# Kernel optimization log

Hardware: AMD Instinct MI355X
Metric: run time of the kernel (lower is better)

Reference implementation:

```python
import jax, jax.numpy as jnp
import numpy as np
import math

D = 256        # input_size == d_k == d_v (per the module: d_k = input_size)
H = 4          # n_heads
MAX_LEN = 800  # PositionalEncoding max_len
NEG = float(-(2**32) + 1)
LN_EPS = 1e-5


def _make_pe():
    pe = np.zeros((MAX_LEN, D), dtype=np.float32)
    pos = np.arange(MAX_LEN, dtype=np.float32)[:, None]
    div = np.exp(np.arange(0, D, 2, dtype=np.float32) * -(math.log(10000.0) / D))
    pe[:, 0::2] = np.sin(pos * div)
    pe[:, 1::2] = np.cos(pos * div)
    return jnp.asarray(pe)


def setup_inputs() -> dict:
    key = jax.random.key(0)
    ks = jax.random.split(key, 12)
    B, L = 32, 512

    def xavier(k, shape):
        fan_in, fan_out = shape[0], shape[1]
        std = math.sqrt(2.0 / (fan_in + fan_out))
        return jax.random.normal(k, shape, dtype=jnp.float32) * std

    return {
        "Q": jax.random.normal(ks[0], (B, L, D), dtype=jnp.float32),
        "K": jax.random.normal(ks[1], (B, L, D), dtype=jnp.float32),
        "V": jax.random.normal(ks[2], (B, L, D), dtype=jnp.float32),
        "mask": jax.random.randint(ks[3], (B, L), 0, 2).astype(jnp.bool_),
        "pe": _make_pe(),
        "W_q": xavier(ks[4], (D, H * D)),
        "W_k": xavier(ks[5], (D, H * D)),
        "W_v": xavier(ks[6], (D, H * D)),
        "W_o": xavier(ks[7], (H * D, D)),
        "w1": xavier(ks[8], (D, D)),
        "b1": jnp.zeros((D,), dtype=jnp.float32),
        "w2": xavier(ks[9], (D, D)),
        "b2": jnp.zeros((D,), dtype=jnp.float32),
        "gamma": jnp.ones((D,), dtype=jnp.float32),
        "beta": jnp.zeros((D,), dtype=jnp.float32),
    }


def _layer_norm(x, gamma, beta):
    mu = jnp.mean(x, axis=-1, keepdims=True)
    var = jnp.mean(jnp.square(x - mu), axis=-1, keepdims=True)
    return (x - mu) * jax.lax.rsqrt(var + LN_EPS) * gamma + beta


def _mha(Q, K, V, mask, W_q, W_k, W_v, W_o):
    B, Lq, _ = Q.shape
    Lk = K.shape[1]

    def split_heads(X, W, L):
        # (B, L, D) @ (D, H*D) -> (B*H, L, D)
        return (X @ W).reshape(B, L, H, D).transpose(0, 2, 1, 3).reshape(B * H, L, D)

    Qh = split_heads(Q, W_q, Lq)
    Kh = split_heads(K, W_k, Lk)
    Vh = split_heads(V, W_v, Lk)

    scale = D ** 0.5 + 1e-6
    scores = jnp.einsum('bqd,bkd->bqk', Qh, Kh) / scale  # (B*H, Lq, Lk)

    pad = jnp.broadcast_to(mask[:, None, :], (B, H, Lq)).reshape(B * H, Lq)
    pad_mask = jnp.broadcast_to(pad[:, :, None], (B * H, Lq, Lk))
    causal = jnp.triu(jnp.ones((Lq, Lk), dtype=jnp.bool_), k=1)
    full_mask = causal[None] | pad_mask
    scores = jnp.where(full_mask, NEG, scores)

    att = jax.nn.softmax(scores, axis=-1)
    Vatt = jnp.einsum('bqk,bkd->bqd', att, Vh)  # (B*H, Lq, D)
    Vatt = Vatt.reshape(B, H, Lq, D).transpose(0, 2, 1, 3).reshape(B, Lq, H * D)
    return Vatt @ W_o


def reference(Q, K, V, mask, pe, W_q, W_k, W_v, W_o, w1, b1, w2, b2, gamma, beta):
    Lq, Lk, Lv = Q.shape[1], K.shape[1], V.shape[1]
    Qp = Q + pe[None, :Lq]
    Kp = K + pe[None, :Lk]
    Vp = V + pe[None, :Lv]

    Vatt = _mha(Qp, Kp, Vp, mask, W_q, W_k, W_v, W_o)
    X = _layer_norm(Qp + Vatt, gamma, beta)
    ffn = jax.nn.relu(X @ w1.T + b1) @ w2.T + b2
    return _layer_norm(ffn + X, gamma, beta)
```

## Files before the change

kernel.cpp:

```cpp
#include <hip/hip_runtime.h>
#include <stdint.h>

#define SEQ   512
#define DM    256
#define NB    32
#define NH    4
#define HD    (NH * DM)
#define PE_MASK (SEQ * DM - 1)
#define NEGV  (-4294967295.0f)

typedef __attribute__((ext_vector_type(8))) short short8;
typedef __attribute__((ext_vector_type(4))) float f32x4;

#if defined(__has_builtin)
#if __has_builtin(__builtin_amdgcn_global_load_lds)
#define HAS_ASYNC 1
#endif
#endif
#ifndef HAS_ASYNC
#define HAS_ASYNC 0
#endif

__device__ __forceinline__ float b2f(unsigned short u) {
    return __uint_as_float(((uint32_t)u) << 16);
}
__device__ __forceinline__ unsigned short f2b(float f) {
    uint32_t u = __float_as_uint(f);
    u += 0x7fffu + ((u >> 16) & 1u);
    return (unsigned short)(u >> 16);
}

__global__ __launch_bounds__(256) void mask_canon(
    const unsigned char* __restrict__ raw, int* __restrict__ canon)
{
    __shared__ int enc_byte, enc_odd;
    int tid = threadIdx.x;
    if (tid == 0) { enc_byte = 0; enc_odd = 0; }
    __syncthreads();
    if (tid < 255 && raw[tid * 4 + 1]) atomicOr(&enc_byte, 1);
    if (tid < 128 && ((const int*)raw)[tid * 2 + 1]) atomicOr(&enc_odd, 1);
    __syncthreads();
    int i = blockIdx.x * 256 + tid;
    int v;
    if (enc_byte)      v = (raw[i] != 0);
    else if (enc_odd)  v = (((const int*)raw)[i] != 0);
    else               v = ((((const int*)raw)[i * 2] | ((const int*)raw)[i * 2 + 1]) != 0);
    canon[i] = v;
}

__global__ __launch_bounds__(256) void addpe3(
    const float* __restrict__ Q, const float* __restrict__ K,
    const float* __restrict__ V, const float* __restrict__ pe,
    unsigned short* __restrict__ Qp, unsigned short* __restrict__ Kp,
    unsigned short* __restrict__ Vp)
{
    int blk = blockIdx.x;
    int seg = blk >> 12;
    const float* X = (seg == 0) ? Q : (seg == 1) ? K : V;
    unsigned short* O = (seg == 0) ? Qp : (seg == 1) ? Kp : Vp;
    long i = (long)((blk & 4095) * 256 + threadIdx.x) * 4;
    float4 x = *reinterpret_cast<const float4*>(X + i);
    float4 p = *reinterpret_cast<const float4*>(pe + (i & PE_MASK));
    ushort4 o;
    o.x = f2b(x.x + p.x); o.y = f2b(x.y + p.y);
    o.z = f2b(x.z + p.z); o.w = f2b(x.w + p.w);
    *reinterpret_cast<ushort4*>(O + i) = o;
}

__global__ __launch_bounds__(256) void conv2(
    const float* __restrict__ w1, const float* __restrict__ w2,
    unsigned short* __restrict__ o1, unsigned short* __restrict__ o2)
{
    int blk = blockIdx.x;
    const float* in = (blk < 64) ? w1 : w2;
    unsigned short* out = (blk < 64) ? o1 : o2;
    long i = (long)((blk & 63) * 256 + threadIdx.x) * 4;
    float4 x = *reinterpret_cast<const float4*>(in + i);
    ushort4 o;
    o.x = f2b(x.x); o.y = f2b(x.y); o.z = f2b(x.z); o.w = f2b(x.w);
    *reinterpret_cast<ushort4*>(out + i) = o;
}

__global__ __launch_bounds__(256) void transpose_f2b3(
    const float* __restrict__ in0, const float* __restrict__ in1,
    const float* __restrict__ in2, unsigned short* __restrict__ out,
    int ldin, int ldout, long outStride)
{
    int z = blockIdx.z;
    const float* in = (z == 0) ? in0 : (z == 1) ? in1 : in2;
    unsigned short* op = out + z * outStride;
    __shared__ unsigned short tile[32][33];
    int r0 = blockIdx.y * 32, c0 = blockIdx.x * 32;
    int i = threadIdx.x >> 3;
    int j = (threadIdx.x & 7) * 4;
    float4 v = *reinterpret_cast<const float4*>(in + (long)(r0 + i) * ldin + c0 + j);
    tile[i][j + 0] = f2b(v.x); tile[i][j + 1] = f2b(v.y);
    tile[i][j + 2] = f2b(v.z); tile[i][j + 3] = f2b(v.w);
    __syncthreads();
    ushort4 w;
    w.x = tile[j + 0][i]; w.y = tile[j + 1][i]; w.z = tile[j + 2][i]; w.w = tile[j + 3][i];
    *reinterpret_cast<ushort4*>(op + (long)(c0 + i) * ldout + r0 + j) = w;
}

__global__ __launch_bounds__(256) void transpose_f2b(
    const float* __restrict__ in, unsigned short* __restrict__ out,
    int ldin, int ldout)
{
    __shared__ unsigned short tile[32][33];
    int r0 = blockIdx.y * 32, c0 = blockIdx.x * 32;
    int i = threadIdx.x >> 3;
    int j = (threadIdx.x & 7) * 4;
    float4 v = *reinterpret_cast<const float4*>(in + (long)(r0 + i) * ldin + c0 + j);
    tile[i][j + 0] = f2b(v.x); tile[i][j + 1] = f2b(v.y);
    tile[i][j + 2] = f2b(v.z); tile[i][j + 3] = f2b(v.w);
    __syncthreads();
    ushort4 w;
    w.x = tile[j + 0][i]; w.y = tile[j + 1][i]; w.z = tile[j + 2][i]; w.w = tile[j + 3][i];
    *reinterpret_cast<ushort4*>(out + (long)(c0 + i) * ldout + r0 + j) = w;
}

__global__ __launch_bounds__(256) void transpose_bf16(
    const unsigned short* __restrict__ in, unsigned short* __restrict__ out,
    int ldin, int ldout, long sInB, long sInH, long sOutB, long sOutH, int Hdiv)
{
    int z = blockIdx.z; int b = z / Hdiv; int h = z % Hdiv;
    const unsigned short* ip = in + b * sInB + h * sInH;
    unsigned short* op = out + b * sOutB + h * sOutH;
    __shared__ unsigned short tile[32][33];
    int r0 = blockIdx.y * 32, c0 = blockIdx.x * 32;
    int i = threadIdx.x >> 3;
    int j = (threadIdx.x & 7) * 4;
    ushort4 v = *reinterpret_cast<const ushort4*>(ip + (long)(r0 + i) * ldin + c0 + j);
    tile[i][j + 0] = v.x; tile[i][j + 1] = v.y; tile[i][j + 2] = v.z; tile[i][j + 3] = v.w;
    __syncthreads();
    ushort4 w;
    w.x = tile[j + 0][i]; w.y = tile[j + 1][i]; w.z = tile[j + 2][i]; w.w = tile[j + 3][i];
    *reinterpret_cast<ushort4*>(op + (long)(c0 + i) * ldout + r0 + j) = w;
}

template<bool BIAS, bool RELU, bool OUTBF16>
__global__ __launch_bounds__(256) void gemm_bt(
    const unsigned short* __restrict__ A, int lda,
    const unsigned short* __restrict__ B, int ldb,
    void* __restrict__ Cv, int ldc,
    const float* __restrict__ bias, float scale, int K, int Hdiv,
    long sAb, long sAh, long sAz,
    long sBb, long sBh, long sBz,
    long sCb, long sCh, long sCz)
{
    const int m0 = blockIdx.y * 128;
    const int n0 = blockIdx.x * 128;
    int z  = blockIdx.z;
    int bb = z / Hdiv, hh = z % Hdiv;
    const unsigned short* Ab = A + bb * sAb + hh * sAh + (long)z * sAz;
    const unsigned short* Bb = B + bb * sBb + hh * sBh + (long)z * sBz;
    long coff = bb * sCb + hh * sCh + (long)z * sCz;

    __shared__ unsigned short As[128 * 32];
    __shared__ unsigned short Bs[128 * 32];

    const int tid  = threadIdx.x;
    const int lane = tid & 63;
    const int wave = tid >> 6;
    const int wm   = (wave >> 1) * 64;
    const int wn   = (wave & 1) * 64;
    const int lm   = lane & 15;
    const int kq   = (lane >> 4) * 8;

    f32x4 acc[4][4] = {};

    for (int k0 = 0; k0 < K; k0 += 32) {
#pragma unroll
        for (int it = 0; it < 2; ++it) {
            int id = tid + it * 256;
            int r  = id >> 2;
            int c8 = (id & 3) * 8;
            const unsigned short* gA = Ab + (long)(m0 + r) * lda + k0 + c8;
            const unsigned short* gB = Bb + (long)(n0 + r) * ldb + k0 + c8;
#if HAS_ASYNC
            unsigned short* lA = &As[(size_t)(it * 256 + wave * 64) * 8];
            unsigned short* lB = &Bs[(size_t)(it * 256 + wave * 64) * 8];
            __builtin_amdgcn_global_load_lds(
                (const __attribute__((address_space(1))) void*)gA,
                (__attribute__((address_space(3))) void*)lA, 16, 0, 0);
            __builtin_amdgcn_global_load_lds(
                (const __attribute__((address_space(1))) void*)gB,
                (__attribute__((address_space(3))) void*)lB, 16, 0, 0);
#else
            *reinterpret_cast<uint4*>(&As[(size_t)id * 8]) =
                *reinterpret_cast<const uint4*>(gA);
            *reinterpret_cast<uint4*>(&Bs[(size_t)id * 8]) =
                *reinterpret_cast<const uint4*>(gB);
#endif
        }
        __syncthreads();

        short8 af[4], bfr[4];
#pragma unroll
        for (int i = 0; i < 4; ++i)
            af[i] = *reinterpret_cast<const short8*>(&As[(wm + i * 16 + lm) * 32 + kq]);
#pragma unroll
        for (int j = 0; j < 4; ++j)
            bfr[j] = *reinterpret_cast<const short8*>(&Bs[(wn + j * 16 + lm) * 32 + kq]);
#pragma unroll
        for (int i = 0; i < 4; ++i)
#pragma unroll
            for (int j = 0; j < 4; ++j)
                acc[i][j] = __builtin_amdgcn_mfma_f32_16x16x32_bf16(af[i], bfr[j], acc[i][j], 0, 0, 0);
        __syncthreads();
    }

#pragma unroll
    for (int j = 0; j < 4; ++j) {
        int col  = n0 + wn + j * 16 + lm;
        float bv = 0.f;
        if (BIAS) bv = bias[col];
#pragma unroll
        for (int i = 0; i < 4; ++i) {
#pragma unroll
            for (int r = 0; r < 4; ++r) {
                int row = m0 + wm + i * 16 + (lane >> 4) * 4 + r;
                float v = acc[i][j][r] * scale + bv;
                if (RELU) v = fmaxf(v, 0.f);
                long idx = coff + (long)row * ldc + col;
                if (OUTBF16) reinterpret_cast<unsigned short*>(Cv)[idx] = f2b(v);
                else         reinterpret_cast<float*>(Cv)[idx] = v;
            }
        }
    }
}

__global__ __launch_bounds__(256, 3) void flash_attn(
    const unsigned short* __restrict__ Qh,
    const unsigned short* __restrict__ Kh,
    const unsigned short* __restrict__ VhT,
    unsigned short* __restrict__ Vatt,
    const int* __restrict__ maskc, int bh0, float scale, int nbh)
{
    const int tid  = threadIdx.x;
    const int lane = tid & 63;
    const int wave = tid >> 6;
    const int lm   = lane & 15;
    const int qg   = lane >> 4;
    const int kq   = qg * 8;

    const int L = blockIdx.x;
    int z, qt;
    if ((nbh & 7) == 0) {
        int x = L & 7, m = L >> 3;
        qt = m & 7;
        z  = x + 8 * (m >> 3);
    } else {
        z = L % nbh; qt = L / nbh;
    }
    const int b_l = z >> 2, h = z & 3;
    const int m0  = qt * 64;
    const int wq0 = m0 + wave * 16;
    const long qkbase = (long)b_l * SEQ * HD + (long)h * DM;
    const unsigned short* Aq = Qh + qkbase;
    const unsigned short* Ak = Kh + qkbase;
    const unsigned short* Av = VhT + (long)b_l * SEQ * HD + (long)h * SEQ * DM;
    unsigned short* Ov = Vatt + qkbase;
    const int bglob = (bh0 + z) >> 2;

    __shared__ unsigned short Ks[SEQ * 32];
    __shared__ __align__(16) unsigned short Pw[4][16][40];

    f32x4 S[32] = {};
    const int NT = (m0 >> 4) + wave + 1;

    for (int kc = 0; kc < 8; ++kc) {
        for (int it = 0; it <= qt; ++it) {
            int id = tid + it * 256;
            const unsigned short* g = Ak + (long)(id >> 2) * HD + kc * 32 + (id & 3) * 8;
#if HAS_ASYNC
            unsigned short* l = &Ks[(size_t)(it * 256 + wave * 64) * 8];
            __builtin_amdgcn_global_load_lds(
                (const __attribute__((address_space(1))) void*)g,
                (__attribute__((address_space(3))) void*)l, 16, 0, 0);
#else
            *reinterpret_cast<uint4*>(&Ks[(size_t)id * 8]) =
                *reinterpret_cast<const uint4*>(g);
#endif
        }
        short8 qf = *reinterpret_cast<const short8*>(
            Aq + (long)(wq0 + lm) * HD + kc * 32 + kq);
        __syncthreads();
#pragma unroll
        for (int nt = 0; nt < 32; ++nt) {
            if (nt < NT) {
                short8 bf = *reinterpret_cast<const short8*>(&Ks[(nt * 16 + lm) * 32 + kq]);
                S[nt] = __builtin_amdgcn_mfma_f32_16x16x32_bf16(qf, bf, S[nt], 0, 0, 0);
            }
        }
        __syncthreads();
    }

    unsigned short* Vb0 = Ks;
    unsigned short* Vb1 = Ks + 8192;
#pragma unroll
    for (int it = 0; it < 4; ++it) {
        int id = tid + it * 256;
        const unsigned short* g = Av + (long)(id >> 2) * SEQ + (id & 3) * 8;
#if HAS_ASYNC
        unsigned short* l = &Vb0[(size_t)(it * 256 + wave * 64) * 8];
        __builtin_amdgcn_global_load_lds(
            (const __attribute__((address_space(1))) void*)g,
            (__attribute__((address_space(3))) void*)l, 16, 0, 0);
#else
        *reinterpret_cast<uint4*>(&Vb0[(size_t)id * 8]) =
            *reinterpret_cast<const uint4*>(g);
#endif
    }

    int   qrow[4];
    bool  rowm[4];
    float mx[4], sm[4];
#pragma unroll
    for (int r = 0; r < 4; ++r) {
        int q = wq0 + qg * 4 + r;
        qrow[r] = q;
        rowm[r] = maskc[bglob * SEQ + q] != 0;
        mx[r] = -3.4e38f;
    }
#pragma unroll
    for (int nt = 0; nt < 32; ++nt) {
        int k = nt * 16 + lm;
#pragma unroll
        for (int r = 0; r < 4; ++r) {
            float v = S[nt][r] * scale;
            if (k > qrow[r] || rowm[r]) v = NEGV;
            S[nt][r] = v;
            mx[r] = fmaxf(mx[r], v);
        }
    }
#pragma unroll
    for (int r = 0; r < 4; ++r) {
#pragma unroll
        for (int off = 8; off >= 1; off >>= 1)
            mx[r] = fmaxf(mx[r], __shfl_xor(mx[r], off));
        sm[r] = 0.f;
    }
    uint32_t pk[32][2];
#pragma unroll
    for (int nt = 0; nt < 32; ++nt) {
        float e0 = __expf(S[nt][0] - mx[0]);
        float e1 = __expf(S[nt][1] - mx[1]);
        float e2 = __expf(S[nt][2] - mx[2]);
        float e3 = __expf(S[nt][3] - mx[3]);
        sm[0] += e0; sm[1] += e1; sm[2] += e2; sm[3] += e3;
        pk[nt][0] = (uint32_t)f2b(e0) | ((uint32_t)f2b(e1) << 16);
        pk[nt][1] = (uint32_t)f2b(e2) | ((uint32_t)f2b(e3) << 16);
    }
#pragma unroll
    for (int r = 0; r < 4; ++r) {
#pragma unroll
        for (int off = 8; off >= 1; off >>= 1)
            sm[r] += __shfl_xor(sm[r], off);
        sm[r] = 1.0f / sm[r];
    }

    f32x4 O[16] = {};
#pragma unroll
    for (int kc2 = 0; kc2 < 16; ++kc2) {
        unsigned short* Vcur = (kc2 & 1) ? Vb1 : Vb0;
        __syncthreads();
        if (kc2 < 15) {
            unsigned short* Vnext = (kc2 & 1) ? Vb0 : Vb1;
#pragma unroll
            for (int it = 0; it < 4; ++it) {
                int id = tid + it * 256;
                const unsigned short* g =
                    Av + (long)(id >> 2) * SEQ + (kc2 + 1) * 32 + (id & 3) * 8;
#if HAS_ASYNC
                unsigned short* l = &Vnext[(size_t)(it * 256 + wave * 64) * 8];
                __builtin_amdgcn_global_load_lds(
                    (const __attribute__((address_space(1))) void*)g,
                    (__attribute__((address_space(3))) void*)l, 16, 0, 0);
#else
                *reinterpret_cast<uint4*>(&Vnext[(size_t)id * 8]) =
                    *reinterpret_cast<const uint4*>(g);
#endif
            }
        }
#pragma unroll
        for (int t = 0; t < 2; ++t) {
            int nt = kc2 * 2 + t;
#pragma unroll
            for (int r = 0; r < 4; ++r)
                Pw[wave][qg * 4 + r][t * 16 + lm] =
                    (unsigned short)(pk[nt][r >> 1] >> ((r & 1) * 16));
        }
        short8 pf = *reinterpret_cast<const short8*>(&Pw[wave][lm][kq]);
#pragma unroll
        for (int nt2 = 0; nt2 < 16; ++nt2) {
            short8 vf = *reinterpret_cast<const short8*>(&Vcur[(nt2 * 16 + lm) * 32 + kq]);
            O[nt2] = __builtin_amdgcn_mfma_f32_16x16x32_bf16(pf, vf, O[nt2], 0, 0, 0);
        }
    }

#pragma unroll
    for (int nt2 = 0; nt2 < 16; ++nt2) {
#pragma unroll
        for (int r = 0; r < 4; ++r) {
            int l = wq0 + qg * 4 + r;
            Ov[(long)l * HD + nt2 * 16 + lm] = f2b(O[nt2][r] * sm[r]);
        }
    }
}

__global__ __launch_bounds__(256) void ln1_kernel(
    const unsigned short* __restrict__ AttO, const float* __restrict__ Q,
    const float* __restrict__ pe,
    const float* __restrict__ gamma, const float* __restrict__ beta,
    float* __restrict__ outf, unsigned short* __restrict__ outb)
{
    int row  = blockIdx.x * 4 + (threadIdx.x >> 6);
    int lane = threadIdx.x & 63;
    long base = (long)row * DM + lane * 4;
    ushort4 a = *reinterpret_cast<const ushort4*>(AttO + base);
    float4 qv = *reinterpret_cast<const float4*>(Q + base);
    float4 pv = *reinterpret_cast<const float4*>(pe + (base & PE_MASK));
    float x[4] = {b2f(a.x) + qv.x + pv.x, b2f(a.y) + qv.y + pv.y,
                  b2f(a.z) + qv.z + pv.z, b2f(a.w) + qv.w + pv.w};
    float s = x[0] + x[1] + x[2] + x[3];
#pragma unroll
    for (int off = 32; off > 0; off >>= 1) s += __shfl_xor(s, off);
    float mu = s * (1.0f / DM);
    float vs = 0.f;
#pragma unroll
    for (int t = 0; t < 4; ++t) { float d = x[t] - mu; vs += d * d; }
#pragma unroll
    for (int off = 32; off > 0; off >>= 1) vs += __shfl_xor(vs, off);
    float inv = rsqrtf(vs * (1.0f / DM) + 1e-5f);
    int d0 = lane * 4;
    float4 g = *reinterpret_cast<const float4*>(gamma + d0);
    float4 bt = *reinterpret_cast<const float4*>(beta + d0);
    float4 o;
    o.x = (x[0] - mu) * inv * g.x + bt.x;
    o.y = (x[1] - mu) * inv * g.y + bt.y;
    o.z = (x[2] - mu) * inv * g.z + bt.z;
    o.w = (x[3] - mu) * inv * g.w + bt.w;
    *reinterpret_cast<float4*>(outf + base) = o;
    ushort4 ob;
    ob.x = f2b(o.x); ob.y = f2b(o.y); ob.z = f2b(o.z); ob.w = f2b(o.w);
    *reinterpret_cast<ushort4*>(outb + base) = ob;
}

__global__ __launch_bounds__(256) void ln2_kernel(
    const float* __restrict__ F, const float* __restrict__ X,
    const float* __restrict__ gamma, const float* __restrict__ beta,
    float* __restrict__ out)
{
    int row  = blockIdx.x * 4 + (threadIdx.x >> 6);
    int lane = threadIdx.x & 63;
    long base = (long)row * DM + lane * 4;
    float4 a = *reinterpret_cast<const float4*>(F + base);
    float4 c = *reinterpret_cast<const float4*>(X + base);
    float x[4] = {a.x + c.x, a.y + c.y, a.z + c.z, a.w + c.w};
    float s = x[0] + x[1] + x[2] + x[3];
#pragma unroll
    for (int off = 32; off > 0; off >>= 1) s += __shfl_xor(s, off);
    float mu = s * (1.0f / DM);
    float vs = 0.f;
#pragma unroll
    for (int t = 0; t < 4; ++t) { float d = x[t] - mu; vs += d * d; }
#pragma unroll
    for (int off = 32; off > 0; off >>= 1) vs += __shfl_xor(vs, off);
    float inv = rsqrtf(vs * (1.0f / DM) + 1e-5f);
    int d0 = lane * 4;
    float4 g = *reinterpret_cast<const float4*>(gamma + d0);
    float4 bt = *reinterpret_cast<const float4*>(beta + d0);
    float4 o;
    o.x = (x[0] - mu) * inv * g.x + bt.x;
    o.y = (x[1] - mu) * inv * g.y + bt.y;
    o.z = (x[2] - mu) * inv * g.z + bt.z;
    o.w = (x[3] - mu) * inv * g.w + bt.w;
    *reinterpret_cast<float4*>(out + base) = o;
}

extern "C" void kernel_launch(void* const* d_in, const int* in_sizes, int n_in,
                              void* d_out, int out_size, void* d_ws, size_t ws_size,
                              hipStream_t stream)
{
    const float* Q  = (const float*)d_in[0];
    const float* Ki = (const float*)d_in[1];
    const float* Vi = (const float*)d_in[2];
    const unsigned char* mask_raw = (const unsigned char*)d_in[3];
    const float* pe = (const float*)d_in[4];
    const float* Wq = (const float*)d_in[5];
    const float* Wk = (const float*)d_in[6];
    const float* Wv = (const float*)d_in[7];
    const float* Wo = (const float*)d_in[8];
    const float* w1 = (const float*)d_in[9];
    const float* b1 = (const float*)d_in[10];
    const float* w2 = (const float*)d_in[11];
    const float* b2 = (const float*)d_in[12];
    const float* gamma = (const float*)d_in[13];
    const float* beta  = (const float*)d_in[14];
    float* out = (float*)d_out;

    const size_t MiB = 1048576;
    char* ws = (char*)d_ws;

    int CB = 1;
    for (int cb = 32; cb >= 1; cb >>= 1) {
        size_t scr_sz = (size_t)(5 * cb) * MiB;
        if (scr_sz < 24 * MiB) scr_sz = 24 * MiB;
        if ((59 * MiB + scr_sz) <= ws_size) { CB = cb; break; }
    }
    const int NCH = NB / CB;

    unsigned short* WqT  = (unsigned short*)(ws);
    unsigned short* WkT  = WqT + 262144;
    unsigned short* WvT  = WkT + 262144;
    unsigned short* WoT  = WvT + 262144;
    unsigned short* w1b  = (unsigned short*)(ws + 2 * MiB);
    unsigned short* w2b  = w1b + 65536;
    int*            maskc = (int*)(ws + 2 * MiB + 262144);
    unsigned short* Qp   = (unsigned short*)(ws + 3 * MiB);
    unsigned short* Kp   = (unsigned short*)(ws + 11 * MiB);
    unsigned short* Vp   = (unsigned short*)(ws + 19 * MiB);
    unsigned short* AttO = (unsigned short*)(ws + 27 * MiB);
    unsigned short* Xb   = (unsigned short*)(ws + 35 * MiB);
    float*          Xf   = (float*)(ws + 43 * MiB);
    char*           scr  = ws + 59 * MiB;
    unsigned short* Qh   = (unsigned short*)(scr);
    unsigned short* Kh   = (unsigned short*)(scr + (size_t)CB * MiB);
    unsigned short* Vh   = (unsigned short*)(scr + (size_t)2 * CB * MiB);
    unsigned short* VhT  = (unsigned short*)(scr + (size_t)3 * CB * MiB);
    unsigned short* Vatt = (unsigned short*)(scr + (size_t)4 * CB * MiB);
    unsigned short* H1   = (unsigned short*)(scr);
    float*          Ff   = (float*)(scr + 8 * MiB);

    const float scale = (float)(1.0 / (16.0 + 1e-6));
    const long CROWS = (long)CB * SEQ;
    const long CBELT = (long)CB * MiB / 2;

    mask_canon<<<64, 256, 0, stream>>>(mask_raw, maskc);
    transpose_f2b3<<<dim3(32, 8, 3), 256, 0, stream>>>(Wq, Wk, Wv, WqT, HD, DM, 262144);
    transpose_f2b<<<dim3(8, 32, 1), 256, 0, stream>>>(Wo, WoT, DM, HD);
    conv2<<<128, 256, 0, stream>>>(w1, w2, w1b, w2b);
    addpe3<<<12288, 256, 0, stream>>>(Q, Ki, Vi, pe, Qp, Kp, Vp);

    for (int c = 0; c < NCH; ++c) {
        const long r0   = (long)c * CROWS;
        const int  bh0  = c * CB * NH;
        const int  gy   = (int)(CROWS / 128);
        const int  nbh  = CB * NH;

        gemm_bt<false, false, true><<<dim3(8, gy, 3), 256, 0, stream>>>(
            Qp + r0 * DM, DM, WqT, DM, Qh, HD, nullptr, 1.f, DM,
            1, 4194304, 0, 0, 262144, 0, 0, CBELT, 0, 0);

        transpose_bf16<<<dim3(8, 16, CB * NH), 256, 0, stream>>>(
            Vh, VhT, HD, SEQ, (long)SEQ * HD, DM, (long)SEQ * HD, (long)SEQ * DM, NH);

        flash_attn<<<dim3(8 * nbh, 1, 1), 256, 0, stream>>>(
            Qh, Kh, VhT, Vatt, maskc, bh0, scale, nbh);

        gemm_bt<false, false, true><<<dim3(2, gy, 1), 256, 0, stream>>>(
            Vatt, HD, WoT, HD, AttO + r0 * DM, DM, nullptr, 1.f, HD,
            1, 0,0,0, 0,0,0, 0,0,0);
    }

    ln1_kernel<<<4096, 256, 0, stream>>>(AttO, Q, pe, gamma, beta, Xf, Xb);

    gemm_bt<true, true, true><<<dim3(2, 128, 1), 256, 0, stream>>>(
        Xb, DM, w1b, DM, H1, DM, b1, 1.f, DM, 1, 0,0,0, 0,0,0, 0,0,0);
    gemm_bt<true, false, false><<<dim3(2, 128, 1), 256, 0, stream>>>(
        H1, DM, w2b, DM, Ff, DM, b2, 1.f, DM, 1, 0,0,0, 0,0,0, 0,0,0);

    ln2_kernel<<<4096, 256, 0, stream>>>(Ff, Xf, gamma, beta, out);
}
```

Before: 381.7 us.

## Skip causal-masked V tiles and handle padded rows via precomputed V mean

In the PV loop, flash attention now processes only the key chunks up to the query tile's causal limit and no longer walks all 16 chunks. Fully padded query rows, whose softmax over uniform NEG scores is a plain average of V, are skipped in attention. New kernels compute the per-batch V column mean and write it into those rows afterwards. The flash kernel's occupancy hint drops from 3 to 2, and the change adds three small kernel launches plus extra scratch space.

```diff
diff --git a/kernel.cpp b/kernel.cpp
--- a/kernel.cpp
+++ b/kernel.cpp
@@ -136,6 +136,52 @@
     ushort4 w;
     w.x = tile[j + 0][i]; w.y = tile[j + 1][i]; w.z = tile[j + 2][i]; w.w = tile[j + 3][i];
     *reinterpret_cast<ushort4*>(op + (long)(c0 + i) * ldout + r0 + j) = w;
+}
+
+__global__ __launch_bounds__(256) void vmean_part(
+    const unsigned short* __restrict__ Vh, float* __restrict__ part)
+{
+    int bl = blockIdx.x, seg = blockIdx.y;
+    const unsigned short* p = Vh + (long)bl * SEQ * HD + (long)seg * 64 * HD;
+    int c = threadIdx.x * 4;
+    float s0 = 0.f, s1 = 0.f, s2 = 0.f, s3 = 0.f;
+    for (int l = 0; l < 64; ++l) {
+        ushort4 v = *reinterpret_cast<const ushort4*>(p + (long)l * HD + c);
+        s0 += b2f(v.x); s1 += b2f(v.y); s2 += b2f(v.z); s3 += b2f(v.w);
+    }
+    float4 o = {s0, s1, s2, s3};
+    *reinterpret_cast<float4*>(part + (long)(bl * 8 + seg) * HD + c) = o;
+}
+
+__global__ __launch_bounds__(256) void vmean_reduce(
+    const float* __restrict__ part, unsigned short* __restrict__ Vm)
+{
+    int bl = blockIdx.x;
+    int c = threadIdx.x * 4;
+    const float* p = part + (long)bl * 8 * HD + c;
+    float s0 = 0.f, s1 = 0.f, s2 = 0.f, s3 = 0.f;
+#pragma unroll
+    for (int seg = 0; seg < 8; ++seg) {
+        float4 v = *reinterpret_cast<const float4*>(p + (long)seg * HD);
+        s0 += v.x; s1 += v.y; s2 += v.z; s3 += v.w;
+    }
+    const float inv = 1.0f / SEQ;
+    ushort4 o;
+    o.x = f2b(s0 * inv); o.y = f2b(s1 * inv);
+    o.z = f2b(s2 * inv); o.w = f2b(s3 * inv);
+    *reinterpret_cast<ushort4*>(Vm + (long)bl * HD + c) = o;
+}
+
+__global__ __launch_bounds__(256) void fix_mask(
+    const unsigned short* __restrict__ Vm, unsigned short* __restrict__ Vatt,
+    const int* __restrict__ maskc, int b0)
+{
+    int row = blockIdx.x;
+    int bl = row >> 9, l = row & (SEQ - 1);
+    if (maskc[(long)(b0 + bl) * SEQ + l] == 0) return;
+    int c = threadIdx.x * 4;
+    ushort4 v = *reinterpret_cast<const ushort4*>(Vm + (long)bl * HD + c);
+    *reinterpret_cast<ushort4*>(Vatt + (long)row * HD + c) = v;
 }
 
 template<bool BIAS, bool RELU, bool OUTBF16>
@@ -230,7 +276,7 @@
     }
 }
 
-__global__ __launch_bounds__(256, 3) void flash_attn(
+__global__ __launch_bounds__(256, 2) void flash_attn(
     const unsigned short* __restrict__ Qh,
     const unsigned short* __restrict__ Kh,
     const unsigned short* __restrict__ VhT,
@@ -329,7 +375,7 @@
 #pragma unroll
         for (int r = 0; r < 4; ++r) {
             float v = S[nt][r] * scale;
-            if (k > qrow[r] || rowm[r]) v = NEGV;
+            if (k > qrow[r]) v = NEGV;
             S[nt][r] = v;
             mx[r] = fmaxf(mx[r], v);
         }
@@ -360,51 +406,56 @@
         sm[r] = 1.0f / sm[r];
     }
 
+    const int KC = 2 * (qt + 1);
     f32x4 O[16] = {};
 #pragma unroll
     for (int kc2 = 0; kc2 < 16; ++kc2) {
-        unsigned short* Vcur = (kc2 & 1) ? Vb1 : Vb0;
-        __syncthreads();
-        if (kc2 < 15) {
-            unsigned short* Vnext = (kc2 & 1) ? Vb0 : Vb1;
-#pragma unroll
-            for (int it = 0; it < 4; ++it) {
-                int id = tid + it * 256;
-                const unsigned short* g =
-                    Av + (long)(id >> 2) * SEQ + (kc2 + 1) * 32 + (id & 3) * 8;
+        if (kc2 < KC) {
+            unsigned short* Vcur = (kc2 & 1) ? Vb1 : Vb0;
+            __syncthreads();
+            if (kc2 + 1 < KC) {
+                unsigned short* Vnext = (kc2 & 1) ? Vb0 : Vb1;
+#pragma unroll
+                for (int it = 0; it < 4; ++it) {
+                    int id = tid + it * 256;
+                    const unsigned short* g =
+                        Av + (long)(id >> 2) * SEQ + (kc2 + 1) * 32 + (id & 3) * 8;
 #if HAS_ASYNC
-                unsigned short* l = &Vnext[(size_t)(it * 256 + wave * 64) * 8];
-                __builtin_amdgcn_global_load_lds(
-                    (const __attribute__((address_space(1))) void*)g,
-                    (__attribute__((address_space(3))) void*)l, 16, 0, 0);
+                    unsigned short* l = &Vnext[(size_t)(it * 256 + wave * 64) * 8];
+                    __builtin_amdgcn_global_load_lds(
+                        (const __attribute__((address_space(1))) void*)g,
+                        (__attribute__((address_space(3))) void*)l, 16, 0, 0);
 #else
-                *reinterpret_cast<uint4*>(&Vnext[(size_t)id * 8]) =
-                    *reinterpret_cast<const uint4*>(g);
+                    *reinterpret_cast<uint4*>(&Vnext[(size_t)id * 8]) =
+                        *reinterpret_cast<const uint4*>(g);
 #endif
+                }
+            }
+#pragma unroll
+            for (int t = 0; t < 2; ++t) {
+                int nt = kc2 * 2 + t;
+#pragma unroll
+                for (int r = 0; r < 4; ++r)
+                    Pw[wave][qg * 4 + r][t * 16 + lm] =
+                        (unsigned short)(pk[nt][r >> 1] >> ((r & 1) * 16));
+            }
+            short8 pf = *reinterpret_cast<const short8*>(&Pw[wave][lm][kq]);
+#pragma unroll
+            for (int nt2 = 0; nt2 < 16; ++nt2) {
+                short8 vf = *reinterpret_cast<const short8*>(&Vcur[(nt2 * 16 + lm) * 32 + kq]);
+                O[nt2] = __builtin_amdgcn_mfma_f32_16x16x32_bf16(pf, vf, O[nt2], 0, 0, 0);
             }
         }
-#pragma unroll
-        for (int t = 0; t < 2; ++t) {
-            int nt = kc2 * 2 + t;
-#pragma unroll
-            for (int r = 0; r < 4; ++r)
-                Pw[wave][qg * 4 + r][t * 16 + lm] =
-                    (unsigned short)(pk[nt][r >> 1] >> ((r & 1) * 16));
-        }
-        short8 pf = *reinterpret_cast<const short8*>(&Pw[wave][lm][kq]);
-#pragma unroll
-        for (int nt2 = 0; nt2 < 16; ++nt2) {
-            short8 vf = *reinterpret_cast<const short8*>(&Vcur[(nt2 * 16 + lm) * 32 + kq]);
-            O[nt2] = __builtin_amdgcn_mfma_f32_16x16x32_bf16(pf, vf, O[nt2], 0, 0, 0);
-        }
     }
 
 #pragma unroll
     for (int nt2 = 0; nt2 < 16; ++nt2) {
 #pragma unroll
         for (int r = 0; r < 4; ++r) {
-            int l = wq0 + qg * 4 + r;
-            Ov[(long)l * HD + nt2 * 16 + lm] = f2b(O[nt2][r] * sm[r]);
+            if (!rowm[r]) {
+                int l = wq0 + qg * 4 + r;
+                Ov[(long)l * HD + nt2 * 16 + lm] = f2b(O[nt2][r] * sm[r]);
+            }
         }
     }
 }
@@ -505,7 +556,7 @@
 
     int CB = 1;
     for (int cb = 32; cb >= 1; cb >>= 1) {
-        size_t scr_sz = (size_t)(5 * cb) * MiB;
+        size_t scr_sz = (size_t)(5 * cb) * MiB + (size_t)cb * 34816;
         if (scr_sz < 24 * MiB) scr_sz = 24 * MiB;
         if ((59 * MiB + scr_sz) <= ws_size) { CB = cb; break; }
     }
@@ -530,6 +581,9 @@
     unsigned short* Vh   = (unsigned short*)(scr + (size_t)2 * CB * MiB);
     unsigned short* VhT  = (unsigned short*)(scr + (size_t)3 * CB * MiB);
     unsigned short* Vatt = (unsigned short*)(scr + (size_t)4 * CB * MiB);
+    float*          part = (float*)(scr + (size_t)5 * CB * MiB);
+    unsigned short* Vm   = (unsigned short*)(scr + (size_t)5 * CB * MiB
+                                             + (size_t)CB * 8 * HD * 4);
     unsigned short* H1   = (unsigned short*)(scr);
     float*          Ff   = (float*)(scr + 8 * MiB);
 
@@ -556,8 +610,13 @@
         transpose_bf16<<<dim3(8, 16, CB * NH), 256, 0, stream>>>(
             Vh, VhT, HD, SEQ, (long)SEQ * HD, DM, (long)SEQ * HD, (long)SEQ * DM, NH);
 
+        vmean_part<<<dim3(CB, 8), 256, 0, stream>>>(Vh, part);
+        vmean_reduce<<<CB, 256, 0, stream>>>(part, Vm);
+
         flash_attn<<<dim3(8 * nbh, 1, 1), 256, 0, stream>>>(
             Qh, Kh, VhT, Vatt, maskc, bh0, scale, nbh);
+
+        fix_mask<<<(int)CROWS, 256, 0, stream>>>(Vm, Vatt, maskc, c * CB);
 
         gemm_bt<false, false, true><<<dim3(2, gy, 1), 256, 0, stream>>>(
             Vatt, HD, WoT, HD, AttO + r0 * DM, DM, nullptr, 1.f, HD,
```

Result: faster. 351.5 us (-7.9%).
